# Kernel tuning notes

Hardware: AMD Instinct MI355X
Metric: run time of the kernel (lower is better)

## Reference

```python
import jax, jax.numpy as jnp
import numpy as np
from jax.scipy.stats import norm

H, W = 512, 512
HP, WP = 3, 3            # plane window
T_BINS, R_BINS = 180, 360  # accumulator dims (theta, rho)
THR_VAR = 100.0
ORIGIN = (0, 0)


def setup_inputs() -> dict:
    key = jax.random.key(0)
    k1, _ = jax.random.split(key)
    img = jax.random.uniform(k1, (H, W), dtype=jnp.float32)
    mask = jnp.ones((H, W), dtype=jnp.float32)
    return {"img": img, "mask": mask}


def _shift(img, dx, dy):
    # edge-clamped shifted view, matches xi = clip(hi+dx, 0, H-1)
    ri = jnp.clip(jnp.arange(H) + dx, 0, H - 1)
    ci = jnp.clip(jnp.arange(W) + dy, 0, W - 1)
    return img[ri][:, ci]


def reference(img, mask):
    img = img.astype(jnp.float32)
    dxs = range(-(HP // 2), HP // 2 + 1)
    dys = range(-(WP // 2), WP // 2 + 1)
    sum_x2 = float(sum(dx * dx for dx in dxs) * WP)  # = 6 for 3x3
    sum_y2 = float(sum(dy * dy for dy in dys) * HP)
    n_win = float(HP * WP)

    # ---- local plane fit (vectorized over all pixels, loop over 9 offsets) ----
    alpha = jnp.zeros((H, W), jnp.float32)
    beta = jnp.zeros((H, W), jnp.float32)
    gamma = jnp.zeros((H, W), jnp.float32)
    for dx in dxs:
        for dy in dys:
            s = _shift(img, dx, dy)
            alpha = alpha + dx * s
            beta = beta + dy * s
            gamma = gamma + s
    alpha = alpha / sum_x2 + 1e-6
    beta = beta / sum_y2 + 1e-6
    gamma = gamma / n_win

    # ---- residual variance (faithful to source: uses img[xi, wi]) ----
    eps2 = jnp.zeros((H, W), jnp.float32)
    for dx in dxs:
        row_s = _shift(img, dx, 0)  # img[clip(hi+dx), wi]
        for dy in dys:
            r = row_s - alpha * dy - beta * dx - gamma
            eps2 = eps2 + r * r
    noise_var = eps2 / (n_win - 2.0)
    var_alpha = noise_var / sum_x2
    var_beta = noise_var / sum_y2
    covar_ab = jnp.zeros_like(noise_var)  # sum_xy == 0 for symmetric window

    # ---- polar coordinates + uncertainty propagation ----
    theta = jnp.arctan(beta / alpha)  # in (-pi/2, pi/2)
    xg = (jnp.arange(H, dtype=jnp.float32) - ORIGIN[0])[:, None]
    yg = (jnp.arange(W, dtype=jnp.float32) - ORIGIN[1])[None, :]
    ct, st = jnp.cos(theta), jnp.sin(theta)
    rho = xg * ct + yg * st
    g2 = (alpha * alpha + beta * beta)
    var_theta = (beta * beta * var_alpha + alpha * alpha * var_beta
                 - 2.0 * alpha * beta * covar_ab) / (g2 * g2)
    drho_dt = -xg * st + yg * ct
    var_rho = drho_dt * drho_dt * var_theta

    # ---- Gaussian soft-voting into the accumulator ----
    theta_min, theta_max = -np.pi / 2, np.pi / 2
    rho_max = float(np.sqrt(H ** 2 + W ** 2))
    rho_min = -rho_max
    t_bin = (theta_max - theta_min) / (T_BINS - 1)
    r_bin = (rho_max - rho_min) / (R_BINS - 1)
    # bin i covers [center - bin/2, center + bin/2]
    t_edges = theta_min + (jnp.arange(T_BINS + 1, dtype=jnp.float32) - 0.5) * t_bin
    r_edges = rho_min + (jnp.arange(R_BINS + 1, dtype=jnp.float32) - 0.5) * r_bin

    valid = ((var_theta <= THR_VAR) & (var_rho <= THR_VAR)).astype(jnp.float32) * mask

    P = H * W
    thf = theta.reshape(P)
    rhf = rho.reshape(P)
    sig_t = jnp.sqrt(var_theta + 1e-12).reshape(P)
    sig_r = jnp.sqrt(var_rho + 1e-12).reshape(P)
    vf = valid.reshape(P)

    # per-pixel probability mass in each theta / rho bin (marginal Gaussian CDFs)
    cdf_t = norm.cdf((t_edges[None, :] - thf[:, None]) / sig_t[:, None])  # (P, T+1)
    wt = (cdf_t[:, 1:] - cdf_t[:, :-1]) * vf[:, None]                    # (P, T)
    cdf_r = norm.cdf((r_edges[None, :] - rhf[:, None]) / sig_r[:, None])  # (P, R+1)
    wr = cdf_r[:, 1:] - cdf_r[:, :-1]                                     # (P, R)

    acc = jnp.einsum('pt,pr->tr', wt, wr)  # (T_BINS, R_BINS) accumulated votes
    return acc
```

## Files before the change

kernel.cpp:

```cpp
#include <hip/hip_runtime.h>
#include <math.h>

#define H 512
#define W 512
#define TBINS 180
#define RBINS 360
#define NPIX (H*W)

#define THETA_MIN (-1.5707963267948966f)
#define T_BIN ((float)(3.141592653589793 / 179.0))
#define R_MIN (-724.0773439350246f)
#define R_BIN ((float)(2.0 * 724.0773439350246 / 359.0))
#define THR_VAR 100.0f
#define WSIG 6.0f

#define NT 6
#define NBLK 1024
#define SCAP 256
#define MPAD 192
#define GG 512
#define NCKCAP 1024

typedef short v8s __attribute__((ext_vector_type(8)));
typedef float v4f __attribute__((ext_vector_type(4)));

__device__ __forceinline__ float phi_cdf(float z) {
    return 0.5f * erfcf(-0.70710678118654752f * z);
}
__device__ __forceinline__ unsigned short f2bf(float f) {
    unsigned u = __float_as_uint(f);
    return (unsigned short)((u + 0x7FFF + ((u >> 16) & 1)) >> 16);
}
__device__ __forceinline__ float bf2f(unsigned short b) {
    return __uint_as_float(((unsigned)b) << 16);
}

__global__ void prep_kernel(const float* __restrict__ img,
                            const float* __restrict__ mask,
                            int* __restrict__ cblk,
                            float4* __restrict__ recs,
                            float* __restrict__ mvs) {
    __shared__ int lcnt[NT];
    int tid = threadIdx.x;
    int b = blockIdx.x;
    int gid = b * blockDim.x + tid;
    if (tid < NT) lcnt[tid] = 0;
    __syncthreads();

    int p = gid;
    int hi = p >> 9, wi = p & (W - 1);
    float mv = mask[p];

    int xm = max(hi - 1, 0), xp = min(hi + 1, H - 1);
    int ym = max(wi - 1, 0), yp = min(wi + 1, W - 1);
    const float* r0 = img + xm * W;
    const float* r1 = img + hi * W;
    const float* r2 = img + xp * W;
    float s00 = r0[ym], s01 = r0[wi], s02 = r0[yp];
    float s10 = r1[ym], s11 = r1[wi], s12 = r1[yp];
    float s20 = r2[ym], s21 = r2[wi], s22 = r2[yp];

    float alpha_s = (s20 + s21 + s22) - (s00 + s01 + s02);
    float beta_s  = (s02 + s12 + s22) - (s00 + s10 + s20);
    float gsum    = s00 + s01 + s02 + s10 + s11 + s12 + s20 + s21 + s22;

    float alpha = alpha_s * (1.0f / 6.0f) + 1e-6f;
    float beta  = beta_s  * (1.0f / 6.0f) + 1e-6f;
    float gamma = gsum * (1.0f / 9.0f);

    float cvals[3] = { s01, s11, s21 };
    float eps2 = 0.0f;
    #pragma unroll
    for (int ix = 0; ix < 3; ++ix) {
        float dx = (float)(ix - 1);
        float c = cvals[ix];
        #pragma unroll
        for (int iy = 0; iy < 3; ++iy) {
            float dy = (float)(iy - 1);
            float r = c - alpha * dy - beta * dx - gamma;
            eps2 += r * r;
        }
    }
    float noise_var = eps2 * (1.0f / 7.0f);
    float va = noise_var * (1.0f / 6.0f);
    float g2 = alpha * alpha + beta * beta;
    float var_theta = (beta * beta * va + alpha * alpha * va) / (g2 * g2);

    float x = (float)hi, y = (float)wi;
    float inv_g = rsqrtf(g2);
    float cta = fabsf(alpha) * inv_g;
    float sta = (alpha < 0.0f ? -beta : beta) * inv_g;
    float drho_a = -x * sta + y * cta;
    float var_rho_a = drho_a * drho_a * var_theta;
    bool maybe = (var_theta <= THR_VAR) && (var_rho_a <= THR_VAR * 1.01f) && (mv != 0.0f);

    int myNt[2] = { -1, -1 };
    int myPos[2];
    float4 rc;
    if (maybe) {
        float theta = atanf(beta / alpha);
        float ct = cosf(theta), st = sinf(theta);
        float rho = x * ct + y * st;
        float drho = -x * st + y * ct;
        float var_rho = drho * drho * var_theta;
        if (var_rho <= THR_VAR) {
            float sig_t = sqrtf(var_theta + 1e-12f);
            float sig_r = sqrtf(var_rho + 1e-12f);
            float radr = WSIG * sig_r;
            int rlo = max((int)floorf((rho - radr - R_MIN) / R_BIN - 0.5f), 0);
            int rhi = min((int)ceilf((rho + radr - R_MIN) / R_BIN + 0.5f), RBINS - 1);
            if (rhi >= rlo) {
                rc.x = theta; rc.y = 1.0f / sig_t; rc.z = rho; rc.w = 1.0f / sig_r;
                int nt0 = rlo >> 6, nt1 = rhi >> 6;
                for (int nt = nt0; nt <= nt1; ++nt) {
                    int k = nt - nt0;
                    myNt[k] = nt;
                    myPos[k] = atomicAdd(&lcnt[nt], 1);
                }
            }
        }
    }
    __syncthreads();
    if (tid < NT) cblk[tid * NBLK + b] = lcnt[tid];
    #pragma unroll
    for (int k = 0; k < 2; ++k) {
        if (myNt[k] >= 0) {
            int idx = (myNt[k] * NBLK + b) * SCAP + myPos[k];
            recs[idx] = rc;
            mvs[idx]  = mv;
        }
    }
}

__global__ void __launch_bounds__(512)
gemm_kernel(const float4* __restrict__ recs,
            const float* __restrict__ mvs,
            const int* __restrict__ cblk,
            int* __restrict__ ckp_g,
            float* __restrict__ part) {
    __shared__ __align__(16) unsigned short Ah[MPAD * 32], Al[MPAD * 32];
    __shared__ __align__(16) unsigned short Bh[64 * 32],  Bl[64 * 32];
    __shared__ float4 prec[32];
    __shared__ float  pmv[32];
    __shared__ int    pref[NT][NBLK];
    __shared__ int    wsum[8][NT], woff[8][NT];
    __shared__ int    ckp[NT + 1], cnl[NT];

    int tid = threadIdx.x;
    int lane = tid & 63, wv = tid >> 6;
    int nsub = wv & 3, mhalf = wv >> 2;

    int a0[NT], a1[NT], s[NT];
    #pragma unroll
    for (int t = 0; t < NT; ++t) {
        a0[t] = cblk[t * NBLK + 2 * tid];
        a1[t] = cblk[t * NBLK + 2 * tid + 1];
        s[t] = a0[t] + a1[t];
    }
    #pragma unroll
    for (int d = 1; d < 64; d <<= 1) {
        #pragma unroll
        for (int t = 0; t < NT; ++t) {
            int u = __shfl_up(s[t], d);
            if (lane >= d) s[t] += u;
        }
    }
    if (lane == 63) {
        #pragma unroll
        for (int t = 0; t < NT; ++t) wsum[wv][t] = s[t];
    }
    __syncthreads();
    if (tid == 0) {
        #pragma unroll
        for (int t = 0; t < NT; ++t) {
            int r = 0;
            #pragma unroll
            for (int i = 0; i < 8; ++i) { woff[i][t] = r; r += wsum[i][t]; }
        }
    }
    __syncthreads();
    #pragma unroll
    for (int t = 0; t < NT; ++t) {
        int base = woff[wv][t] + s[t];
        pref[t][2 * tid]     = base - a1[t];
        pref[t][2 * tid + 1] = base;
    }
    __syncthreads();
    if (tid == 0) {
        int r = 0;
        #pragma unroll
        for (int t = 0; t < NT; ++t) {
            ckp[t] = min(r, NCKCAP);
            int cn = pref[t][NBLK - 1];
            cnl[t] = cn;
            r += (cn + 31) >> 5;
        }
        ckp[NT] = min(r, NCKCAP);
    }
    __syncthreads();
    if (blockIdx.x == 0 && tid <= NT) ckp_g[tid] = ckp[tid];
    int nchunks = ckp[NT];

    int pix = tid & 31, g = tid >> 5;

    for (int c = blockIdx.x; c < nchunks; c += GG) {
        if (c != (int)blockIdx.x) __syncthreads();

        int t = 0;
        #pragma unroll
        for (int i = 1; i < NT; ++i) if (c >= ckp[i]) t = i;
        int c0 = t * 64;
        int nbmax = min(63, RBINS - 1 - c0);
        int cn = cnl[t];
        int k0 = (c - ckp[t]) << 5;
        int k1 = min(k0 + 32, cn);

        if (tid < 32) {
            int r = k0 + tid;
            float4 rcv; rcv.x = 0.f; rcv.y = 0.f; rcv.z = 0.f; rcv.w = 0.f;
            float m = 0.f;
            if (r < k1) {
                int pos = 0;
                #pragma unroll
                for (int st = 512; st >= 1; st >>= 1)
                    if (pos + st <= NBLK && pref[t][pos + st - 1] <= r) pos += st;
                int off = r - (pos ? pref[t][pos - 1] : 0);
                int idx = (t * NBLK + pos) * SCAP + off;
                rcv = recs[idx]; m = mvs[idx];
            }
            prec[tid] = rcv; pmv[tid] = m;
        }
        __syncthreads();

        {
            float4 rc = prec[pix];
            float m = pmv[pix];
            bool live = (rc.y != 0.0f);
            if (g < 12) {
                int e0 = g << 4;
                float sigt = 1.0f / rc.y;
                int wx = max((int)floorf((rc.x - WSIG * sigt - THETA_MIN) / T_BIN - 0.5f), 0);
                int wy = min((int)ceilf((rc.x + WSIG * sigt - THETA_MIN) / T_BIN + 0.5f), TBINS - 1);
                int sb = e0 * 32 + pix;
                float prev = 0.0f;
                #pragma unroll 1
                for (int i = 0; i <= 16; ++i) {
                    int e = e0 + i;
                    float val;
                    if (!live || e < wx) val = 0.0f;
                    else if (e > wy + 1) val = 1.0f;
                    else {
                        float edge = THETA_MIN + ((float)e - 0.5f) * T_BIN;
                        val = phi_cdf((edge - rc.x) * rc.y);
                    }
                    if (i > 0) {
                        float wt = (val - prev) * m;
                        unsigned short hb = f2bf(wt);
                        Ah[sb + (i - 1) * 32] = hb;
                        Al[sb + (i - 1) * 32] = f2bf(wt - bf2f(hb));
                    }
                    prev = val;
                }
            } else {
                int n0 = (g - 12) << 4;
                float sigr = 1.0f / rc.w;
                int wz = max((int)floorf((rc.z - WSIG * sigr - R_MIN) / R_BIN - 0.5f) - c0, 0);
                int ww = min((int)ceilf((rc.z + WSIG * sigr - R_MIN) / R_BIN + 0.5f) - c0, nbmax);
                int sb = n0 * 32 + pix;
                float prev = 0.0f;
                #pragma unroll 1
                for (int i = 0; i <= 16; ++i) {
                    int n = n0 + i;
                    float val;
                    if (!live || n < wz) val = 0.0f;
                    else if (n > ww + 1) val = 1.0f;
                    else {
                        float edge = R_MIN + ((float)(c0 + n) - 0.5f) * R_BIN;
                        val = phi_cdf((edge - rc.z) * rc.w);
                    }
                    if (i > 0) {
                        float wr = val - prev;
                        unsigned short hb = f2bf(wr);
                        Bh[sb + (i - 1) * 32] = hb;
                        Bl[sb + (i - 1) * 32] = f2bf(wr - bf2f(hb));
                    }
                    prev = val;
                }
            }
        }
        __syncthreads();

        v4f zero = {0.f, 0.f, 0.f, 0.f};
        v4f acc[6];
        #pragma unroll
        for (int i = 0; i < 6; ++i) acc[i] = zero;

        int kq = (lane >> 4) * 8;
        int mr = lane & 15;
        v8s bh = *((__shared__ v8s*)&Bh[(nsub * 16 + mr) * 32 + kq]);
        v8s bl = *((__shared__ v8s*)&Bl[(nsub * 16 + mr) * 32 + kq]);
        #pragma unroll
        for (int mt = 0; mt < 6; ++mt) {
            int mbase = (mhalf * 6 + mt) * 16;
            v8s ah = *((__shared__ v8s*)&Ah[(mbase + mr) * 32 + kq]);
            v8s al = *((__shared__ v8s*)&Al[(mbase + mr) * 32 + kq]);
            acc[mt] = __builtin_amdgcn_mfma_f32_16x16x32_bf16(ah, bh, acc[mt], 0, 0, 0);
            acc[mt] = __builtin_amdgcn_mfma_f32_16x16x32_bf16(ah, bl, acc[mt], 0, 0, 0);
            acc[mt] = __builtin_amdgcn_mfma_f32_16x16x32_bf16(al, bh, acc[mt], 0, 0, 0);
        }

        float* slab = part + (size_t)c * (MPAD * 64);
        int col = nsub * 16 + (lane & 15);
        int rq = (lane >> 4) * 4;
        #pragma unroll
        for (int mt = 0; mt < 6; ++mt) {
            int rbase = (mhalf * 6 + mt) * 16 + rq;
            #pragma unroll
            for (int r = 0; r < 4; ++r)
                slab[(rbase + r) * 64 + col] = acc[mt][r];
        }
    }
}

__global__ void __launch_bounds__(1024)
reduce_kernel(const float4* __restrict__ part, const int* __restrict__ ckp_g,
              float4* __restrict__ out) {
    __shared__ float4 sdata[1024];
    int t = blockIdx.x / 45;
    int tid = threadIdx.x;
    int qi = tid & 63, jg = tid >> 6;
    int q = (blockIdx.x % 45) * 64 + qi;
    int n0 = ckp_g[t], n1 = ckp_g[t + 1];
    float4 s; s.x = 0.f; s.y = 0.f; s.z = 0.f; s.w = 0.f;
    #pragma unroll 4
    for (int j = n0 + jg; j < n1; j += 16) {
        float4 v = part[(size_t)j * (MPAD * 16) + q];
        s.x += v.x; s.y += v.y; s.z += v.z; s.w += v.w;
    }
    sdata[tid] = s;
    __syncthreads();
    #pragma unroll
    for (int h = 8; h >= 1; h >>= 1) {
        if (jg < h) {
            float4 o = sdata[(jg + h) * 64 + qi];
            s.x += o.x; s.y += o.y; s.z += o.z; s.w += o.w;
            sdata[tid] = s;
        }
        __syncthreads();
    }
    if (jg == 0) {
        int row = q >> 4, c4 = q & 15;
        if (!(t == 5 && c4 >= 10))
            out[row * 90 + t * 16 + c4] = s;
    }
}

extern "C" void kernel_launch(void* const* d_in, const int* in_sizes, int n_in,
                              void* d_out, int out_size, void* d_ws, size_t ws_size,
                              hipStream_t stream) {
    const float* img  = (const float*)d_in[0];
    const float* mask = (const float*)d_in[1];
    float4* out = (float4*)d_out;

    char* ws = (char*)d_ws;
    size_t off_recs = 32768;
    size_t off_mvs  = off_recs + (size_t)NT * NBLK * SCAP * 16;
    size_t off_ckp  = off_mvs + (size_t)NT * NBLK * SCAP * 4;
    size_t off_part = off_ckp + 1024;

    int*    cblk = (int*)ws;
    float4* recs = (float4*)(ws + off_recs);
    float*  mvs  = (float*)(ws + off_mvs);
    int*    ckp  = (int*)(ws + off_ckp);
    float*  part = (float*)(ws + off_part);

    prep_kernel<<<NPIX / 256, 256, 0, stream>>>(img, mask, cblk, recs, mvs);
    gemm_kernel<<<GG, 512, 0, stream>>>(recs, mvs, cblk, ckp, part);
    reduce_kernel<<<270, 1024, 0, stream>>>((const float4*)part, ckp, (float4*)out);
}
```

Measured before the change: 81.09 us.

## Fuse partial-sum reduction into GEMM kernel via global atomic completion barrier

```diff
diff --git a/kernel.cpp b/kernel.cpp
--- a/kernel.cpp
+++ b/kernel.cpp
@@ -20,6 +20,7 @@
 #define MPAD 192
 #define GG 512
 #define NCKCAP 1024
+#define RBLK 270
 
 typedef short v8s __attribute__((ext_vector_type(8)));
 typedef float v4f __attribute__((ext_vector_type(4)));
@@ -39,11 +40,13 @@
                             const float* __restrict__ mask,
                             int* __restrict__ cblk,
                             float4* __restrict__ recs,
-                            float* __restrict__ mvs) {
+                            float* __restrict__ mvs,
+                            int* __restrict__ fin) {
     __shared__ int lcnt[NT];
     int tid = threadIdx.x;
     int b = blockIdx.x;
     int gid = b * blockDim.x + tid;
+    if (b == 0 && tid == 0) *fin = 0;
     if (tid < NT) lcnt[tid] = 0;
     __syncthreads();
 
@@ -132,12 +135,13 @@
     }
 }
 
-__global__ void __launch_bounds__(512)
-gemm_kernel(const float4* __restrict__ recs,
-            const float* __restrict__ mvs,
-            const int* __restrict__ cblk,
-            int* __restrict__ ckp_g,
-            float* __restrict__ part) {
+__global__ void __launch_bounds__(512, 4)
+gemmred_kernel(const float4* __restrict__ recs,
+               const float* __restrict__ mvs,
+               const int* __restrict__ cblk,
+               int* __restrict__ fin,
+               float* __restrict__ part,
+               float4* __restrict__ out) {
     __shared__ __align__(16) unsigned short Ah[MPAD * 32], Al[MPAD * 32];
     __shared__ __align__(16) unsigned short Bh[64 * 32],  Bl[64 * 32];
     __shared__ float4 prec[32];
@@ -145,7 +149,9 @@
     __shared__ int    pref[NT][NBLK];
     __shared__ int    wsum[8][NT], woff[8][NT];
     __shared__ int    ckp[NT + 1], cnl[NT];
-
+    __shared__ float4 sdata[512];
+
+    int bid = blockIdx.x;
     int tid = threadIdx.x;
     int lane = tid & 63, wv = tid >> 6;
     int nsub = wv & 3, mhalf = wv >> 2;
@@ -198,13 +204,12 @@
         ckp[NT] = min(r, NCKCAP);
     }
     __syncthreads();
-    if (blockIdx.x == 0 && tid <= NT) ckp_g[tid] = ckp[tid];
     int nchunks = ckp[NT];
 
     int pix = tid & 31, g = tid >> 5;
 
-    for (int c = blockIdx.x; c < nchunks; c += GG) {
-        if (c != (int)blockIdx.x) __syncthreads();
+    for (int c = bid; c < nchunks; c += GG) {
+        if (c != bid) __syncthreads();
 
         int t = 0;
         #pragma unroll
@@ -320,38 +325,49 @@
                 slab[(rbase + r) * 64 + col] = acc[mt][r];
         }
     }
-}
-
-__global__ void __launch_bounds__(1024)
-reduce_kernel(const float4* __restrict__ part, const int* __restrict__ ckp_g,
-              float4* __restrict__ out) {
-    __shared__ float4 sdata[1024];
-    int t = blockIdx.x / 45;
-    int tid = threadIdx.x;
-    int qi = tid & 63, jg = tid >> 6;
-    int q = (blockIdx.x % 45) * 64 + qi;
-    int n0 = ckp_g[t], n1 = ckp_g[t + 1];
-    float4 s; s.x = 0.f; s.y = 0.f; s.z = 0.f; s.w = 0.f;
-    #pragma unroll 4
-    for (int j = n0 + jg; j < n1; j += 16) {
-        float4 v = part[(size_t)j * (MPAD * 16) + q];
-        s.x += v.x; s.y += v.y; s.z += v.z; s.w += v.w;
-    }
-    sdata[tid] = s;
-    __syncthreads();
-    #pragma unroll
-    for (int h = 8; h >= 1; h >>= 1) {
-        if (jg < h) {
-            float4 o = sdata[(jg + h) * 64 + qi];
-            s.x += o.x; s.y += o.y; s.z += o.z; s.w += o.w;
-            sdata[tid] = s;
-        }
+
+    __syncthreads();
+    if (tid == 0) {
+        __threadfence();
+        __hip_atomic_fetch_add(fin, 1, __ATOMIC_RELAXED, __HIP_MEMORY_SCOPE_AGENT);
+    }
+    if (bid >= RBLK) return;
+
+    if (tid == 0) {
+        while (__hip_atomic_load(fin, __ATOMIC_RELAXED, __HIP_MEMORY_SCOPE_AGENT) < GG)
+            __builtin_amdgcn_s_sleep(8);
+        __threadfence();
+    }
+    __syncthreads();
+
+    {
+        int t = bid / 45, qc = bid % 45;
+        int qi = tid & 63, jg = tid >> 6;
+        int q = qc * 64 + qi;
+        int n0 = ckp[t], n1 = ckp[t + 1];
+        const float4* p4 = (const float4*)part;
+        float4 sv; sv.x = 0.f; sv.y = 0.f; sv.z = 0.f; sv.w = 0.f;
+        #pragma unroll 4
+        for (int j = n0 + jg; j < n1; j += 8) {
+            float4 v = p4[(size_t)j * (MPAD * 16) + q];
+            sv.x += v.x; sv.y += v.y; sv.z += v.z; sv.w += v.w;
+        }
+        sdata[tid] = sv;
         __syncthreads();
-    }
-    if (jg == 0) {
-        int row = q >> 4, c4 = q & 15;
-        if (!(t == 5 && c4 >= 10))
-            out[row * 90 + t * 16 + c4] = s;
+        #pragma unroll
+        for (int h = 4; h >= 1; h >>= 1) {
+            if (jg < h) {
+                float4 o = sdata[(jg + h) * 64 + qi];
+                sv.x += o.x; sv.y += o.y; sv.z += o.z; sv.w += o.w;
+                sdata[tid] = sv;
+            }
+            __syncthreads();
+        }
+        if (jg == 0) {
+            int row = q >> 4, c4 = q & 15;
+            if (!(t == 5 && c4 >= 10))
+                out[row * 90 + t * 16 + c4] = sv;
+        }
     }
 }
 
@@ -365,16 +381,15 @@
     char* ws = (char*)d_ws;
     size_t off_recs = 32768;
     size_t off_mvs  = off_recs + (size_t)NT * NBLK * SCAP * 16;
-    size_t off_ckp  = off_mvs + (size_t)NT * NBLK * SCAP * 4;
-    size_t off_part = off_ckp + 1024;
+    size_t off_fin  = off_mvs + (size_t)NT * NBLK * SCAP * 4;
+    size_t off_part = off_fin + 1024;
 
     int*    cblk = (int*)ws;
     float4* recs = (float4*)(ws + off_recs);
     float*  mvs  = (float*)(ws + off_mvs);
-    int*    ckp  = (int*)(ws + off_ckp);
+    int*    fin  = (int*)(ws + off_fin);
     float*  part = (float*)(ws + off_part);
 
-    prep_kernel<<<NPIX / 256, 256, 0, stream>>>(img, mask, cblk, recs, mvs);
-    gemm_kernel<<<GG, 512, 0, stream>>>(recs, mvs, cblk, ckp, part);
-    reduce_kernel<<<270, 1024, 0, stream>>>((const float4*)part, ckp, (float4*)out);
-}
+    prep_kernel<<<NPIX / 256, 256, 0, stream>>>(img, mask, cblk, recs, mvs, fin);
+    gemmred_kernel<<<GG, 512, 0, stream>>>(recs, mvs, cblk, fin, part, out);
+}
```

Measured after the change: 112.4 us. +38.6%, slower.
